# Optimization experiments

Measured on AMD Instinct MI355X. Metric: run time of the kernel, lower is better.

Reference implementation:

```python
import jax, jax.numpy as jnp
import numpy as np

N = 100000      # nodes
E = 1200000     # edges
G = 2048        # graphs in batch
FIN, H, FOUT, K = 75, 16, 64, 3  # in/hidden/out channels, num_stacks


def setup_inputs() -> dict:
    key = jax.random.key(0)
    ks = jax.random.split(key, 12)
    s = 0.1
    return {
        "x": jax.random.normal(ks[0], (N, FIN), jnp.float32),
        "edge_index": jax.random.randint(ks[1], (2, E), 0, N),
        "batch": jnp.sort(jax.random.randint(ks[2], (N,), 0, G)),
        # ARMAConv1 (75 -> 16), shared weights across T=2 layers
        "w1_init": jax.random.normal(ks[3], (K, FIN, H), jnp.float32) * s,
        "w1_w": jax.random.normal(ks[4], (K, H, H), jnp.float32) * s,
        "w1_root": jax.random.normal(ks[5], (K, FIN, H), jnp.float32) * s,
        "w1_bias": jnp.zeros((K, 1, H), jnp.float32),
        # ARMAConv2 (16 -> 64), act=None
        "w2_init": jax.random.normal(ks[6], (K, H, FOUT), jnp.float32) * s,
        "w2_w": jax.random.normal(ks[7], (K, FOUT, FOUT), jnp.float32) * s,
        "w2_root": jax.random.normal(ks[8], (K, H, FOUT), jnp.float32) * s,
        "w2_bias": jnp.zeros((K, 1, FOUT), jnp.float32),
        # gather head Linear(64, 1)
        "wg": jax.random.normal(ks[9], (FOUT, 1), jnp.float32) * s,
        "bg": jnp.zeros((1,), jnp.float32),
    }


def reference(x, edge_index, batch, w1_init, w1_w, w1_root, w1_bias,
              w2_init, w2_w, w2_root, w2_bias, wg, bg):
    row, col = edge_index[0], edge_index[1]
    # gcn_norm without self-loops: deg over target nodes, sym normalization
    deg = jnp.zeros((N,), x.dtype).at[col].add(1.0)
    dinv = jnp.where(deg > 0, deg ** -0.5, 0.0)
    norm = dinv[row] * dinv[col]  # [E]

    def prop(h):  # h: [K, N, F] -> A_norm @ h per stack
        msg = h[:, row, :] * norm[None, :, None]        # [K, E, F]
        return jnp.zeros_like(h).at[:, col, :].add(msg)

    def arma(x0, wi, ww, wr, b, act):
        # x0: [N, Fin]; T=2 layers, shared weights
        out = None
        for t in range(2):
            if t == 0:
                out = jnp.einsum('nf,kfo->kno', x0, wi)   # init transform
            else:
                out = jnp.einsum('kno,kop->knp', out, ww)  # shared weight
            out = prop(out)
            out = out + jnp.einsum('nf,kfo->kno', x0, wr) + b  # root + bias
            if act:
                out = jax.nn.relu(out)
        return out.mean(axis=0)  # average over K stacks -> [N, F]

    h1 = jax.nn.relu(arma(x, w1_init, w1_w, w1_root, w1_bias, True))
    h2 = arma(h1, w2_init, w2_w, w2_root, w2_bias, False)
    # global_add_pool over graph ids, then linear head
    pooled = jnp.zeros((G, h2.shape[-1]), h2.dtype).at[batch].add(h2)
    return pooled @ wg + bg  # [G, 1]
```

## Files before the change

### kernel.cpp

```cpp
#include <hip/hip_runtime.h>

#define NN 100000
#define NE 1200000
#define NG 2048
#define NBK 391
#define CAPQ 4096
#define CAPE 5120

static inline int cdiv(long long a, int b) { return (int)((a + b - 1) / b); }

__device__ __forceinline__ unsigned short f2bf(float f) {
    unsigned int u = __float_as_uint(f);
    u += 0x7fffu + ((u >> 16) & 1u);
    return (unsigned short)(u >> 16);
}
__device__ __forceinline__ unsigned int pack2(float a, float b) {
    return (unsigned int)f2bf(a) | ((unsigned int)f2bf(b) << 16);
}
__device__ __forceinline__ float lo2f(unsigned int w) { return __uint_as_float(w << 16); }
__device__ __forceinline__ float hi2f(unsigned int w) { return __uint_as_float(w & 0xffff0000u); }

__global__ void k_init(int* __restrict__ gcur, uint4* __restrict__ A16,
                       uint4* __restrict__ B16, float2* __restrict__ s12,
                       float* __restrict__ t2, float* __restrict__ dinv) {
    int g = blockIdx.x * blockDim.x + threadIdx.x;
    if (g < NBK) gcur[g] = g * CAPQ;
    if (g == NBK) dinv[NN] = 0.f;
    if (g == NBK + 1) s12[NN] = make_float2(0.f, 0.f);
    if (g == NBK + 2) t2[NN] = 0.f;
    uint4 z = make_uint4(0u, 0u, 0u, 0u);
    int s = g - 512;
    if (s >= 0 && s < 6) {
        A16[(size_t)NN * 6 + s] = z;
        B16[(size_t)NN * 6 + s] = z;
    }
}

__global__ __launch_bounds__(256) void k_part(const int4* __restrict__ row4,
                                              const int4* __restrict__ col4,
                                              int* __restrict__ gcur,
                                              int* __restrict__ pairs, int E4) {
    __shared__ int hcnt[NBK];
    __shared__ int hbase[NBK];
    int chunk = (E4 + gridDim.x - 1) / gridDim.x;
    int beg = blockIdx.x * chunk;
    int end = min(E4, beg + chunk);
    for (int j = threadIdx.x; j < NBK; j += 256) hcnt[j] = 0;
    __syncthreads();
    for (int g = beg + threadIdx.x; g < end; g += 256) {
        int4 c = col4[g];
        atomicAdd(&hcnt[c.x >> 8], 1);
        atomicAdd(&hcnt[c.y >> 8], 1);
        atomicAdd(&hcnt[c.z >> 8], 1);
        atomicAdd(&hcnt[c.w >> 8], 1);
    }
    __syncthreads();
    for (int j = threadIdx.x; j < NBK; j += 256) {
        int c = hcnt[j];
        hbase[j] = c > 0 ? atomicAdd(&gcur[j], c) : 0;
        hcnt[j] = 0;
    }
    __syncthreads();
    for (int g = beg + threadIdx.x; g < end; g += 256) {
        int4 c = col4[g];
        int4 r = row4[g];
        int b0 = c.x >> 8, b1 = c.y >> 8, b2 = c.z >> 8, b3 = c.w >> 8;
        int p0 = hbase[b0] + atomicAdd(&hcnt[b0], 1);
        if (p0 < (b0 + 1) * CAPQ) pairs[p0] = ((c.x & 255) << 17) | r.x;
        int p1 = hbase[b1] + atomicAdd(&hcnt[b1], 1);
        if (p1 < (b1 + 1) * CAPQ) pairs[p1] = ((c.y & 255) << 17) | r.y;
        int p2 = hbase[b2] + atomicAdd(&hcnt[b2], 1);
        if (p2 < (b2 + 1) * CAPQ) pairs[p2] = ((c.z & 255) << 17) | r.z;
        int p3 = hbase[b3] + atomicAdd(&hcnt[b3], 1);
        if (p3 < (b3 + 1) * CAPQ) pairs[p3] = ((c.w & 255) << 17) | r.w;
    }
}

__global__ __launch_bounds__(256) void k_bucket(const int* __restrict__ pairs,
                                                const int* __restrict__ gcur,
                                                int* __restrict__ esrc,
                                                int* __restrict__ rowptrp,
                                                float* __restrict__ dinv, int N) {
    __shared__ int stage[CAPE];
    __shared__ int lcnt[256];
    __shared__ int s[256];
    __shared__ int tot;
    int b = blockIdx.x;
    int base = b << 8;
    int nn = min(256, N - base);
    int qb = b * CAPQ;
    int qe = min(gcur[b], qb + CAPQ);
    int cnt = qe - qb;
    int n4 = cnt >> 2, tail = cnt & 3;
    const int4* pairs4 = (const int4*)(pairs + qb);
    int tid = threadIdx.x;
    lcnt[tid] = 0;
    __syncthreads();
    for (int g = tid; g < n4; g += 256) {
        int4 v = pairs4[g];
        atomicAdd(&lcnt[v.x >> 17], 1);
        atomicAdd(&lcnt[v.y >> 17], 1);
        atomicAdd(&lcnt[v.z >> 17], 1);
        atomicAdd(&lcnt[v.w >> 17], 1);
    }
    if (tid < tail) atomicAdd(&lcnt[pairs[qb + n4 * 4 + tid] >> 17], 1);
    __syncthreads();
    int c = lcnt[tid];
    int pc = (c + 3) & ~3;
    s[tid] = pc;
    __syncthreads();
    for (int off = 1; off < 256; off <<= 1) {
        int t = (tid >= off) ? s[tid - off] : 0;
        __syncthreads();
        s[tid] += t;
        __syncthreads();
    }
    int myofs = s[tid] - pc;
    if (tid == 255) tot = s[255];
    __syncthreads();
    int padded = tot;
    if (tid < nn) {
        dinv[base + tid] = c > 0 ? rsqrtf((float)c) : 0.f;
        rowptrp[base + tid] = ((b * CAPE + myofs) >> 2) | ((pc >> 2) << 20);
    }
    int4* stage4 = (int4*)stage;
    int pad4 = padded >> 2;
    int4 sent = make_int4(N, N, N, N);
    for (int i = tid; i < pad4; i += 256) stage4[i] = sent;
    lcnt[tid] = myofs;
    __syncthreads();
    for (int g = tid; g < n4; g += 256) {
        int4 v = pairs4[g];
        int pos;
        pos = atomicAdd(&lcnt[v.x >> 17], 1); stage[pos] = v.x & 0x1FFFF;
        pos = atomicAdd(&lcnt[v.y >> 17], 1); stage[pos] = v.y & 0x1FFFF;
        pos = atomicAdd(&lcnt[v.z >> 17], 1); stage[pos] = v.z & 0x1FFFF;
        pos = atomicAdd(&lcnt[v.w >> 17], 1); stage[pos] = v.w & 0x1FFFF;
    }
    if (tid < tail) {
        int v = pairs[qb + n4 * 4 + tid];
        int pos = atomicAdd(&lcnt[v >> 17], 1);
        stage[pos] = v & 0x1FFFF;
    }
    __syncthreads();
    int4* esrc4 = (int4*)(esrc + b * CAPE);
    for (int i = tid; i < pad4; i += 256) esrc4[i] = stage4[i];
}

__global__ void k_mmAR(const float* __restrict__ x,
                       const float* __restrict__ w1i, const float* __restrict__ w1r,
                       const float* __restrict__ b1, const float* __restrict__ dinv,
                       ushort4* __restrict__ A16s, float4* __restrict__ R4, int N) {
    __shared__ float4 Wi[900];
    __shared__ float4 Wr[900];
    __shared__ float4 Bs[12];
    const float4* wi4 = (const float4*)w1i;
    const float4* wr4 = (const float4*)w1r;
    for (int i = threadIdx.x; i < 900; i += blockDim.x) { Wi[i] = wi4[i]; Wr[i] = wr4[i]; }
    if (threadIdx.x < 12) Bs[threadIdx.x] = ((const float4*)b1)[threadIdx.x];
    __syncthreads();
    const int total = N * 12;
    const int stride = gridDim.x * blockDim.x;
    for (int idx = blockIdx.x * blockDim.x + threadIdx.x; idx < total; idx += stride) {
        int n = idx / 12;
        int q = idx - n * 12;
        int k = q >> 2, o4 = q & 3;
        const float* xp = x + (size_t)n * 75;
        const float4* wpi = Wi + (k * 75) * 4 + o4;
        const float4* wpr = Wr + (k * 75) * 4 + o4;
        float aix = 0.f, aiy = 0.f, aiz = 0.f, aiw = 0.f;
        float4 br = Bs[q];
        float arx = br.x, ary = br.y, arz = br.z, arw = br.w;
#pragma unroll
        for (int f = 0; f < 75; ++f) {
            float xv = xp[f];
            float4 wi = wpi[f * 4];
            float4 wr = wpr[f * 4];
            aix = fmaf(xv, wi.x, aix);
            aiy = fmaf(xv, wi.y, aiy);
            aiz = fmaf(xv, wi.z, aiz);
            aiw = fmaf(xv, wi.w, aiw);
            arx = fmaf(xv, wr.x, arx);
            ary = fmaf(xv, wr.y, ary);
            arz = fmaf(xv, wr.z, arz);
            arw = fmaf(xv, wr.w, arw);
        }
        float dn = dinv[n];
        ushort4 sa;
        sa.x = f2bf(aix * dn); sa.y = f2bf(aiy * dn);
        sa.z = f2bf(aiz * dn); sa.w = f2bf(aiw * dn);
        A16s[(size_t)n * 12 + q] = sa;
        R4[idx] = make_float4(arx, ary, arz, arw);
    }
}

#define ACC8(W)                                                     \
    a0 += lo2f(W.x); a1 += hi2f(W.x); a2 += lo2f(W.y); a3 += hi2f(W.y); \
    a4 += lo2f(W.z); a5 += hi2f(W.z); a6 += lo2f(W.w); a7 += hi2f(W.w);

template <int HAS_R, int COMPUTE_S, int SCALE_OUT>
__global__ void k_prop48(const uint4* __restrict__ src, const float4* __restrict__ R4,
                         const int* __restrict__ rowptrp, const int* __restrict__ esrc,
                         const float* __restrict__ dinv, float* __restrict__ sv,
                         uint4* __restrict__ dst, int N) {
    const int total = N * 6;
    const int stride = gridDim.x * blockDim.x;
    for (int idx = blockIdx.x * blockDim.x + threadIdx.x; idx < total; idx += stride) {
        int n = idx / 6;
        int q = idx - n * 6;
        int rp = rowptrp[n];
        int beg = (rp & 0xFFFFF) << 2;
        int end = beg + ((rp >> 20) << 2);
        float a0 = 0.f, a1 = 0.f, a2 = 0.f, a3 = 0.f, a4 = 0.f, a5 = 0.f, a6 = 0.f, a7 = 0.f;
        float sd = 0.f;
        int p = beg;
        for (; p + 8 <= end; p += 8) {
            int4 e0 = *(const int4*)(esrc + p);
            int4 e1 = *(const int4*)(esrc + p + 4);
            uint4 w0 = src[(size_t)e0.x * 6 + q];
            uint4 w1 = src[(size_t)e0.y * 6 + q];
            uint4 w2 = src[(size_t)e0.z * 6 + q];
            uint4 w3 = src[(size_t)e0.w * 6 + q];
            uint4 w4 = src[(size_t)e1.x * 6 + q];
            uint4 w5 = src[(size_t)e1.y * 6 + q];
            uint4 w6 = src[(size_t)e1.z * 6 + q];
            uint4 w7 = src[(size_t)e1.w * 6 + q];
            ACC8(w0); ACC8(w1); ACC8(w2); ACC8(w3);
            ACC8(w4); ACC8(w5); ACC8(w6); ACC8(w7);
            if (COMPUTE_S) {
                if (q == 0)
                    sd += ((dinv[e0.x] + dinv[e0.y]) + (dinv[e0.z] + dinv[e0.w]))
                        + ((dinv[e1.x] + dinv[e1.y]) + (dinv[e1.z] + dinv[e1.w]));
            }
        }
        if (p < end) {
            int4 e = *(const int4*)(esrc + p);
            uint4 w0 = src[(size_t)e.x * 6 + q];
            uint4 w1 = src[(size_t)e.y * 6 + q];
            uint4 w2 = src[(size_t)e.z * 6 + q];
            uint4 w3 = src[(size_t)e.w * 6 + q];
            ACC8(w0); ACC8(w1); ACC8(w2); ACC8(w3);
            if (COMPUTE_S) {
                if (q == 0)
                    sd += (dinv[e.x] + dinv[e.y]) + (dinv[e.z] + dinv[e.w]);
            }
        }
        float dn = dinv[n];
        float v0 = a0 * dn, v1 = a1 * dn, v2 = a2 * dn, v3 = a3 * dn;
        float v4 = a4 * dn, v5 = a5 * dn, v6 = a6 * dn, v7 = a7 * dn;
        if (HAS_R) {
            float4 r0 = R4[(size_t)n * 12 + q * 2];
            float4 r1 = R4[(size_t)n * 12 + q * 2 + 1];
            v0 = fmaxf(v0 + r0.x, 0.f); v1 = fmaxf(v1 + r0.y, 0.f);
            v2 = fmaxf(v2 + r0.z, 0.f); v3 = fmaxf(v3 + r0.w, 0.f);
            v4 = fmaxf(v4 + r1.x, 0.f); v5 = fmaxf(v5 + r1.y, 0.f);
            v6 = fmaxf(v6 + r1.z, 0.f); v7 = fmaxf(v7 + r1.w, 0.f);
        }
        if (SCALE_OUT) {
            v0 *= dn; v1 *= dn; v2 *= dn; v3 *= dn;
            v4 *= dn; v5 *= dn; v6 *= dn; v7 *= dn;
        }
        uint4 o;
        o.x = pack2(v0, v1); o.y = pack2(v2, v3);
        o.z = pack2(v4, v5); o.w = pack2(v6, v7);
        dst[(size_t)n * 6 + q] = o;
        if (COMPUTE_S) {
            if (q == 0) sv[n] = sd * dn;
        }
    }
}

__global__ void k_post1(const uint4* __restrict__ A16, const float4* __restrict__ R4,
                        const float* __restrict__ w1w, const float* __restrict__ dinv,
                        const float* __restrict__ u,
                        float* __restrict__ z0, float2* __restrict__ s12, int N) {
    __shared__ float4 Ws[192];
    const float4* w4 = (const float4*)w1w;
    for (int i = threadIdx.x; i < 192; i += blockDim.x) Ws[i] = w4[i];
    __syncthreads();
    const int total = N * 4;
    const int stride = gridDim.x * blockDim.x;
    for (int idx = blockIdx.x * blockDim.x + threadIdx.x; idx < total; idx += stride) {
        int n = idx >> 2;
        int o4 = idx & 3;
        const uint4* ap = A16 + (size_t)n * 6;
        float av[48];
#pragma unroll
        for (int c6 = 0; c6 < 6; ++c6) {
            uint4 w = ap[c6];
            av[c6 * 8 + 0] = lo2f(w.x); av[c6 * 8 + 1] = hi2f(w.x);
            av[c6 * 8 + 2] = lo2f(w.y); av[c6 * 8 + 3] = hi2f(w.y);
            av[c6 * 8 + 4] = lo2f(w.z); av[c6 * 8 + 5] = hi2f(w.z);
            av[c6 * 8 + 6] = lo2f(w.w); av[c6 * 8 + 7] = hi2f(w.w);
        }
        float4 sum = make_float4(0.f, 0.f, 0.f, 0.f);
#pragma unroll
        for (int k = 0; k < 3; ++k) {
            float4 d = R4[(size_t)n * 12 + k * 4 + o4];
#pragma unroll
            for (int i = 0; i < 16; ++i) {
                float a = av[k * 16 + i];
                float4 w = Ws[(k * 16 + i) * 4 + o4];
                d.x = fmaf(a, w.x, d.x);
                d.y = fmaf(a, w.y, d.y);
                d.z = fmaf(a, w.z, d.z);
                d.w = fmaf(a, w.w, d.w);
            }
            d.x = fmaxf(d.x, 0.f); d.y = fmaxf(d.y, 0.f);
            d.z = fmaxf(d.z, 0.f); d.w = fmaxf(d.w, 0.f);
            sum.x += d.x; sum.y += d.y; sum.z += d.z; sum.w += d.w;
        }
        const float third = 1.0f / 3.0f;
        sum.x *= third; sum.y *= third; sum.z *= third; sum.w *= third;
        float4 u0q = ((const float4*)u)[o4];
        float4 u1q = ((const float4*)u)[4 + o4];
        float4 u2q = ((const float4*)u)[8 + o4];
        float d0 = sum.x * u0q.x + sum.y * u0q.y + sum.z * u0q.z + sum.w * u0q.w;
        float d1 = sum.x * u1q.x + sum.y * u1q.y + sum.z * u1q.z + sum.w * u1q.w;
        float d2 = sum.x * u2q.x + sum.y * u2q.y + sum.z * u2q.z + sum.w * u2q.w;
        d0 += __shfl_down(d0, 2, 4); d0 += __shfl_down(d0, 1, 4);
        d1 += __shfl_down(d1, 2, 4); d1 += __shfl_down(d1, 1, 4);
        d2 += __shfl_down(d2, 2, 4); d2 += __shfl_down(d2, 1, 4);
        if (o4 == 0) {
            float dn = dinv[n];
            z0[n] = d0;
            s12[n] = make_float2(d1 * dn, d2 * dn);
        }
    }
}

__global__ void k_passA(const float2* __restrict__ s12,
                        const int* __restrict__ rowptrp, const int* __restrict__ esrc,
                        const float* __restrict__ dinv, const float* __restrict__ z0,
                        float* __restrict__ z01, float* __restrict__ t2, int N) {
    int n = blockIdx.x * blockDim.x + threadIdx.x;
    if (n >= N) return;
    int rp = rowptrp[n];
    int beg = (rp & 0xFFFFF) << 2;
    int end = beg + ((rp >> 20) << 2);
    float S1 = 0.f, S2 = 0.f;
    int p = beg;
    for (; p + 8 <= end; p += 8) {
        int4 e0 = *(const int4*)(esrc + p);
        int4 e1 = *(const int4*)(esrc + p + 4);
        float2 v0 = s12[e0.x], v1 = s12[e0.y], v2 = s12[e0.z], v3 = s12[e0.w];
        float2 v4 = s12[e1.x], v5 = s12[e1.y], v6 = s12[e1.z], v7 = s12[e1.w];
        S1 += ((v0.x + v1.x) + (v2.x + v3.x)) + ((v4.x + v5.x) + (v6.x + v7.x));
        S2 += ((v0.y + v1.y) + (v2.y + v3.y)) + ((v4.y + v5.y) + (v6.y + v7.y));
    }
    if (p < end) {
        int4 e = *(const int4*)(esrc + p);
        float2 v0 = s12[e.x], v1 = s12[e.y], v2 = s12[e.z], v3 = s12[e.w];
        S1 += (v0.x + v1.x) + (v2.x + v3.x);
        S2 += (v0.y + v1.y) + (v2.y + v3.y);
    }
    float dn = dinv[n];
    z01[n] = z0[n] + dn * S1;
    t2[n] = dn * dn * S2;
}

__global__ void k_passB(const float* __restrict__ t2,
                        const int* __restrict__ rowptrp, const int* __restrict__ esrc,
                        const float* __restrict__ dinv, const float* __restrict__ z01,
                        const float* __restrict__ sv, const float* __restrict__ u,
                        const int* __restrict__ batch, float* __restrict__ out, int N) {
    int n = blockIdx.x * blockDim.x + threadIdx.x;
    if (n >= N) return;
    int rp = rowptrp[n];
    int beg = (rp & 0xFFFFF) << 2;
    int end = beg + ((rp >> 20) << 2);
    float S = 0.f;
    int p = beg;
    for (; p + 8 <= end; p += 8) {
        int4 e0 = *(const int4*)(esrc + p);
        int4 e1 = *(const int4*)(esrc + p + 4);
        S += ((t2[e0.x] + t2[e0.y]) + (t2[e0.z] + t2[e0.w]))
           + ((t2[e1.x] + t2[e1.y]) + (t2[e1.z] + t2[e1.w]));
    }
    if (p < end) {
        int4 e = *(const int4*)(esrc + p);
        S += (t2[e.x] + t2[e.y]) + (t2[e.z] + t2[e.w]);
    }
    float v = z01[n] + dinv[n] * S + sv[n] * u[48] + u[49];
    atomicAdd(&out[batch[n]], v);
}

__global__ void k_comb(const float* __restrict__ w2i, const float* __restrict__ w2w,
                       const float* __restrict__ w2r, const float* __restrict__ b2,
                       const float* __restrict__ wg, const float* __restrict__ bg,
                       float* __restrict__ u, float* __restrict__ out) {
    if (blockIdx.x > 0) {
        int g = (blockIdx.x - 1) * 256 + threadIdx.x;
        if (g < NG) out[g] = bg[0];
        return;
    }
    __shared__ float t[3][64];
    int tid = threadIdx.x;
    if (tid < 64) {
#pragma unroll
        for (int k = 0; k < 3; ++k) {
            float a = 0.f;
            for (int j = 0; j < 64; ++j) a = fmaf(w2w[k * 4096 + tid * 64 + j], wg[j], a);
            t[k][tid] = a;
        }
    }
    __syncthreads();
    if (tid < 64) {
        float wgv = wg[tid];
        float tk0 = t[0][tid], tk1 = t[1][tid], tk2 = t[2][tid];
        const float third = 1.0f / 3.0f;
        for (int j = 0; j < 16; ++j) {
            float wi0 = w2i[j * 64 + tid], wi1 = w2i[1024 + j * 64 + tid], wi2 = w2i[2048 + j * 64 + tid];
            float wr0 = w2r[j * 64 + tid], wr1 = w2r[1024 + j * 64 + tid], wr2 = w2r[2048 + j * 64 + tid];
            float a2 = wi0 * tk0 + wi1 * tk1 + wi2 * tk2;
            float a1 = wr0 * tk0 + wr1 * tk1 + wr2 * tk2;
            float a0 = (wr0 + wr1 + wr2) * wgv;
#pragma unroll
            for (int off = 32; off > 0; off >>= 1) {
                a2 += __shfl_down(a2, off, 64);
                a1 += __shfl_down(a1, off, 64);
                a0 += __shfl_down(a0, off, 64);
            }
            if (tid == 0) {
                u[j] = a0 * third;
                u[16 + j] = a1 * third;
                u[32 + j] = a2 * third;
            }
        }
        float b0 = b2[tid], b1v = b2[64 + tid], b2v = b2[128 + tid];
        float c0 = b0 * tk0 + b1v * tk1 + b2v * tk2;
        float c1 = (b0 + b1v + b2v) * wgv;
#pragma unroll
        for (int off = 32; off > 0; off >>= 1) {
            c0 += __shfl_down(c0, off, 64);
            c1 += __shfl_down(c1, off, 64);
        }
        if (tid == 0) {
            u[48] = c0 * third;
            u[49] = c1 * third;
        }
    }
}

extern "C" void kernel_launch(void* const* d_in, const int* in_sizes, int n_in,
                              void* d_out, int out_size, void* d_ws, size_t ws_size,
                              hipStream_t stream) {
    const float* x   = (const float*)d_in[0];
    const int*   ei  = (const int*)d_in[1];
    const int*   batch = (const int*)d_in[2];
    const float* w1i = (const float*)d_in[3];
    const float* w1w = (const float*)d_in[4];
    const float* w1r = (const float*)d_in[5];
    const float* w1b = (const float*)d_in[6];
    const float* w2i = (const float*)d_in[7];
    const float* w2w = (const float*)d_in[8];
    const float* w2r = (const float*)d_in[9];
    const float* w2b = (const float*)d_in[10];
    const float* wg  = (const float*)d_in[11];
    const float* bg  = (const float*)d_in[12];
    float* out = (float*)d_out;

    uint4*  A16  = (uint4*)d_ws;
    uint4*  B16  = A16 + (size_t)(NN + 1) * 6;
    float*  R    = (float*)(B16 + (size_t)(NN + 1) * 6);
    float2* s12  = (float2*)(R + (size_t)NN * 48);
    float*  t2   = (float*)(s12 + NN + 1);
    float*  z0   = t2 + NN + 1;
    float*  z01  = z0 + NN;
    float*  dinv = z01 + NN;
    float*  sv   = dinv + NN + 1;
    float*  u    = sv + NN;
    int* rowptrp = (int*)(u + 64);
    int* gcur    = rowptrp + NN;
    int* pairs   = gcur + 512;
    int* esrc    = pairs + (size_t)(NBK + 1) * CAPQ;

    const int T = 256;

    k_init<<<3, T, 0, stream>>>(gcur, A16, B16, s12, t2, dinv);
    k_part<<<512, T, 0, stream>>>((const int4*)ei, (const int4*)(ei + NE),
                                  gcur, pairs, NE / 4);
    k_bucket<<<NBK, T, 0, stream>>>(pairs, gcur, esrc, rowptrp, dinv, NN);

    k_comb<<<9, T, 0, stream>>>(w2i, w2w, w2r, w2b, wg, bg, u, out);

    k_mmAR<<<2048, T, 0, stream>>>(x, w1i, w1r, w1b, dinv, (ushort4*)A16, (float4*)R, NN);

    k_prop48<1, 1, 1><<<cdiv((long long)NN * 6, T), T, 0, stream>>>(
        A16, (const float4*)R, rowptrp, esrc, dinv, sv, B16, NN);
    k_prop48<0, 0, 0><<<cdiv((long long)NN * 6, T), T, 0, stream>>>(
        B16, nullptr, rowptrp, esrc, dinv, nullptr, A16, NN);
    k_post1<<<cdiv((long long)NN * 4, T), T, 0, stream>>>(
        A16, (const float4*)R, w1w, dinv, u, z0, s12, NN);

    k_passA<<<cdiv(NN, T), T, 0, stream>>>(s12, rowptrp, esrc, dinv, z0, z01, t2, NN);
    k_passB<<<cdiv(NN, T), T, 0, stream>>>(t2, rowptrp, esrc, dinv, z01, sv, u, batch, out, NN);
}
```

Before: 203.0 us.

## Store root term in bf16 and fuse second propagation with post-transform

```diff
diff --git a/kernel.cpp b/kernel.cpp
--- a/kernel.cpp
+++ b/kernel.cpp
@@ -6,6 +6,7 @@
 #define NBK 391
 #define CAPQ 4096
 #define CAPE 5120
+#define NPB 42
 
 static inline int cdiv(long long a, int b) { return (int)((a + b - 1) / b); }
 
@@ -14,8 +15,8 @@
     u += 0x7fffu + ((u >> 16) & 1u);
     return (unsigned short)(u >> 16);
 }
-__device__ __forceinline__ unsigned int pack2(float a, float b) {
-    return (unsigned int)f2bf(a) | ((unsigned int)f2bf(b) << 16);
+__device__ __forceinline__ float bf2f(unsigned short h) {
+    return __uint_as_float((unsigned int)h << 16);
 }
 __device__ __forceinline__ float lo2f(unsigned int w) { return __uint_as_float(w << 16); }
 __device__ __forceinline__ float hi2f(unsigned int w) { return __uint_as_float(w & 0xffff0000u); }
@@ -150,7 +151,7 @@
 __global__ void k_mmAR(const float* __restrict__ x,
                        const float* __restrict__ w1i, const float* __restrict__ w1r,
                        const float* __restrict__ b1, const float* __restrict__ dinv,
-                       ushort4* __restrict__ A16s, float4* __restrict__ R4, int N) {
+                       ushort4* __restrict__ A16s, ushort4* __restrict__ R16s, int N) {
     __shared__ float4 Wi[900];
     __shared__ float4 Wr[900];
     __shared__ float4 Bs[12];
@@ -190,7 +191,10 @@
         sa.x = f2bf(aix * dn); sa.y = f2bf(aiy * dn);
         sa.z = f2bf(aiz * dn); sa.w = f2bf(aiw * dn);
         A16s[(size_t)n * 12 + q] = sa;
-        R4[idx] = make_float4(arx, ary, arz, arw);
+        ushort4 sr;
+        sr.x = f2bf(arx); sr.y = f2bf(ary);
+        sr.z = f2bf(arz); sr.w = f2bf(arw);
+        R16s[(size_t)n * 12 + q] = sr;
     }
 }
 
@@ -198,8 +202,7 @@
     a0 += lo2f(W.x); a1 += hi2f(W.x); a2 += lo2f(W.y); a3 += hi2f(W.y); \
     a4 += lo2f(W.z); a5 += hi2f(W.z); a6 += lo2f(W.w); a7 += hi2f(W.w);
 
-template <int HAS_R, int COMPUTE_S, int SCALE_OUT>
-__global__ void k_prop48(const uint4* __restrict__ src, const float4* __restrict__ R4,
+__global__ void k_prop48(const uint4* __restrict__ src, const uint4* __restrict__ R16,
                          const int* __restrict__ rowptrp, const int* __restrict__ esrc,
                          const float* __restrict__ dinv, float* __restrict__ sv,
                          uint4* __restrict__ dst, int N) {
@@ -227,11 +230,9 @@
             uint4 w7 = src[(size_t)e1.w * 6 + q];
             ACC8(w0); ACC8(w1); ACC8(w2); ACC8(w3);
             ACC8(w4); ACC8(w5); ACC8(w6); ACC8(w7);
-            if (COMPUTE_S) {
-                if (q == 0)
-                    sd += ((dinv[e0.x] + dinv[e0.y]) + (dinv[e0.z] + dinv[e0.w]))
-                        + ((dinv[e1.x] + dinv[e1.y]) + (dinv[e1.z] + dinv[e1.w]));
-            }
+            if (q == 0)
+                sd += ((dinv[e0.x] + dinv[e0.y]) + (dinv[e0.z] + dinv[e0.w]))
+                    + ((dinv[e1.x] + dinv[e1.y]) + (dinv[e1.z] + dinv[e1.w]));
         }
         if (p < end) {
             int4 e = *(const int4*)(esrc + p);
@@ -240,91 +241,118 @@
             uint4 w2 = src[(size_t)e.z * 6 + q];
             uint4 w3 = src[(size_t)e.w * 6 + q];
             ACC8(w0); ACC8(w1); ACC8(w2); ACC8(w3);
-            if (COMPUTE_S) {
-                if (q == 0)
-                    sd += (dinv[e.x] + dinv[e.y]) + (dinv[e.z] + dinv[e.w]);
+            if (q == 0)
+                sd += (dinv[e.x] + dinv[e.y]) + (dinv[e.z] + dinv[e.w]);
+        }
+        float dn = dinv[n];
+        uint4 r = R16[(size_t)n * 6 + q];
+        float v0 = fmaxf(a0 * dn + lo2f(r.x), 0.f) * dn;
+        float v1 = fmaxf(a1 * dn + hi2f(r.x), 0.f) * dn;
+        float v2 = fmaxf(a2 * dn + lo2f(r.y), 0.f) * dn;
+        float v3 = fmaxf(a3 * dn + hi2f(r.y), 0.f) * dn;
+        float v4 = fmaxf(a4 * dn + lo2f(r.z), 0.f) * dn;
+        float v5 = fmaxf(a5 * dn + hi2f(r.z), 0.f) * dn;
+        float v6 = fmaxf(a6 * dn + lo2f(r.w), 0.f) * dn;
+        float v7 = fmaxf(a7 * dn + hi2f(r.w), 0.f) * dn;
+        uint4 o;
+        o.x = (unsigned)f2bf(v0) | ((unsigned)f2bf(v1) << 16);
+        o.y = (unsigned)f2bf(v2) | ((unsigned)f2bf(v3) << 16);
+        o.z = (unsigned)f2bf(v4) | ((unsigned)f2bf(v5) << 16);
+        o.w = (unsigned)f2bf(v6) | ((unsigned)f2bf(v7) << 16);
+        dst[(size_t)n * 6 + q] = o;
+        if (q == 0) sv[n] = sd * dn;
+    }
+}
+
+__global__ __launch_bounds__(256) void k_proppost(
+    const uint4* __restrict__ B16, const ushort4* __restrict__ R16s,
+    const float* __restrict__ w1w, const int* __restrict__ rowptrp,
+    const int* __restrict__ esrc, const float* __restrict__ dinv,
+    const float* __restrict__ u, float* __restrict__ z0,
+    float2* __restrict__ s12, int N) {
+    __shared__ float4 Ws[192];
+    __shared__ float ash[NPB][48];
+    const float4* w4 = (const float4*)w1w;
+    for (int i = threadIdx.x; i < 192; i += 256) Ws[i] = w4[i];
+    int t = threadIdx.x;
+    int nbase = blockIdx.x * NPB;
+    if (t < NPB * 6) {
+        int ln = t / 6, q = t - ln * 6;
+        int n = nbase + ln;
+        if (n < N) {
+            int rp = rowptrp[n];
+            int beg = (rp & 0xFFFFF) << 2;
+            int end = beg + ((rp >> 20) << 2);
+            float a0 = 0.f, a1 = 0.f, a2 = 0.f, a3 = 0.f, a4 = 0.f, a5 = 0.f, a6 = 0.f, a7 = 0.f;
+            int p = beg;
+            for (; p + 8 <= end; p += 8) {
+                int4 e0 = *(const int4*)(esrc + p);
+                int4 e1 = *(const int4*)(esrc + p + 4);
+                uint4 w0 = B16[(size_t)e0.x * 6 + q];
+                uint4 w1 = B16[(size_t)e0.y * 6 + q];
+                uint4 w2 = B16[(size_t)e0.z * 6 + q];
+                uint4 w3 = B16[(size_t)e0.w * 6 + q];
+                uint4 w4v = B16[(size_t)e1.x * 6 + q];
+                uint4 w5 = B16[(size_t)e1.y * 6 + q];
+                uint4 w6 = B16[(size_t)e1.z * 6 + q];
+                uint4 w7 = B16[(size_t)e1.w * 6 + q];
+                ACC8(w0); ACC8(w1); ACC8(w2); ACC8(w3);
+                ACC8(w4v); ACC8(w5); ACC8(w6); ACC8(w7);
             }
-        }
-        float dn = dinv[n];
-        float v0 = a0 * dn, v1 = a1 * dn, v2 = a2 * dn, v3 = a3 * dn;
-        float v4 = a4 * dn, v5 = a5 * dn, v6 = a6 * dn, v7 = a7 * dn;
-        if (HAS_R) {
-            float4 r0 = R4[(size_t)n * 12 + q * 2];
-            float4 r1 = R4[(size_t)n * 12 + q * 2 + 1];
-            v0 = fmaxf(v0 + r0.x, 0.f); v1 = fmaxf(v1 + r0.y, 0.f);
-            v2 = fmaxf(v2 + r0.z, 0.f); v3 = fmaxf(v3 + r0.w, 0.f);
-            v4 = fmaxf(v4 + r1.x, 0.f); v5 = fmaxf(v5 + r1.y, 0.f);
-            v6 = fmaxf(v6 + r1.z, 0.f); v7 = fmaxf(v7 + r1.w, 0.f);
-        }
-        if (SCALE_OUT) {
-            v0 *= dn; v1 *= dn; v2 *= dn; v3 *= dn;
-            v4 *= dn; v5 *= dn; v6 *= dn; v7 *= dn;
-        }
-        uint4 o;
-        o.x = pack2(v0, v1); o.y = pack2(v2, v3);
-        o.z = pack2(v4, v5); o.w = pack2(v6, v7);
-        dst[(size_t)n * 6 + q] = o;
-        if (COMPUTE_S) {
-            if (q == 0) sv[n] = sd * dn;
-        }
-    }
-}
-
-__global__ void k_post1(const uint4* __restrict__ A16, const float4* __restrict__ R4,
-                        const float* __restrict__ w1w, const float* __restrict__ dinv,
-                        const float* __restrict__ u,
-                        float* __restrict__ z0, float2* __restrict__ s12, int N) {
-    __shared__ float4 Ws[192];
-    const float4* w4 = (const float4*)w1w;
-    for (int i = threadIdx.x; i < 192; i += blockDim.x) Ws[i] = w4[i];
-    __syncthreads();
-    const int total = N * 4;
-    const int stride = gridDim.x * blockDim.x;
-    for (int idx = blockIdx.x * blockDim.x + threadIdx.x; idx < total; idx += stride) {
-        int n = idx >> 2;
-        int o4 = idx & 3;
-        const uint4* ap = A16 + (size_t)n * 6;
-        float av[48];
+            if (p < end) {
+                int4 e = *(const int4*)(esrc + p);
+                uint4 w0 = B16[(size_t)e.x * 6 + q];
+                uint4 w1 = B16[(size_t)e.y * 6 + q];
+                uint4 w2 = B16[(size_t)e.z * 6 + q];
+                uint4 w3 = B16[(size_t)e.w * 6 + q];
+                ACC8(w0); ACC8(w1); ACC8(w2); ACC8(w3);
+            }
+            float dn = dinv[n];
+            float* ap = &ash[ln][q * 8];
+            ap[0] = a0 * dn; ap[1] = a1 * dn; ap[2] = a2 * dn; ap[3] = a3 * dn;
+            ap[4] = a4 * dn; ap[5] = a5 * dn; ap[6] = a6 * dn; ap[7] = a7 * dn;
+        }
+    }
+    __syncthreads();
+    if (t < NPB * 4) {
+        int ln = t >> 2, o4 = t & 3;
+        int n = nbase + ln;
+        if (n < N) {
+            float4 sum = make_float4(0.f, 0.f, 0.f, 0.f);
 #pragma unroll
-        for (int c6 = 0; c6 < 6; ++c6) {
-            uint4 w = ap[c6];
-            av[c6 * 8 + 0] = lo2f(w.x); av[c6 * 8 + 1] = hi2f(w.x);
-            av[c6 * 8 + 2] = lo2f(w.y); av[c6 * 8 + 3] = hi2f(w.y);
-            av[c6 * 8 + 4] = lo2f(w.z); av[c6 * 8 + 5] = hi2f(w.z);
-            av[c6 * 8 + 6] = lo2f(w.w); av[c6 * 8 + 7] = hi2f(w.w);
-        }
-        float4 sum = make_float4(0.f, 0.f, 0.f, 0.f);
+            for (int k = 0; k < 3; ++k) {
+                ushort4 rq = R16s[(size_t)n * 12 + k * 4 + o4];
+                float4 d;
+                d.x = bf2f(rq.x); d.y = bf2f(rq.y); d.z = bf2f(rq.z); d.w = bf2f(rq.w);
 #pragma unroll
-        for (int k = 0; k < 3; ++k) {
-            float4 d = R4[(size_t)n * 12 + k * 4 + o4];
-#pragma unroll
-            for (int i = 0; i < 16; ++i) {
-                float a = av[k * 16 + i];
-                float4 w = Ws[(k * 16 + i) * 4 + o4];
-                d.x = fmaf(a, w.x, d.x);
-                d.y = fmaf(a, w.y, d.y);
-                d.z = fmaf(a, w.z, d.z);
-                d.w = fmaf(a, w.w, d.w);
+                for (int i = 0; i < 16; ++i) {
+                    float a = ash[ln][k * 16 + i];
+                    float4 w = Ws[(k * 16 + i) * 4 + o4];
+                    d.x = fmaf(a, w.x, d.x);
+                    d.y = fmaf(a, w.y, d.y);
+                    d.z = fmaf(a, w.z, d.z);
+                    d.w = fmaf(a, w.w, d.w);
+                }
+                d.x = fmaxf(d.x, 0.f); d.y = fmaxf(d.y, 0.f);
+                d.z = fmaxf(d.z, 0.f); d.w = fmaxf(d.w, 0.f);
+                sum.x += d.x; sum.y += d.y; sum.z += d.z; sum.w += d.w;
             }
-            d.x = fmaxf(d.x, 0.f); d.y = fmaxf(d.y, 0.f);
-            d.z = fmaxf(d.z, 0.f); d.w = fmaxf(d.w, 0.f);
-            sum.x += d.x; sum.y += d.y; sum.z += d.z; sum.w += d.w;
-        }
-        const float third = 1.0f / 3.0f;
-        sum.x *= third; sum.y *= third; sum.z *= third; sum.w *= third;
-        float4 u0q = ((const float4*)u)[o4];
-        float4 u1q = ((const float4*)u)[4 + o4];
-        float4 u2q = ((const float4*)u)[8 + o4];
-        float d0 = sum.x * u0q.x + sum.y * u0q.y + sum.z * u0q.z + sum.w * u0q.w;
-        float d1 = sum.x * u1q.x + sum.y * u1q.y + sum.z * u1q.z + sum.w * u1q.w;
-        float d2 = sum.x * u2q.x + sum.y * u2q.y + sum.z * u2q.z + sum.w * u2q.w;
-        d0 += __shfl_down(d0, 2, 4); d0 += __shfl_down(d0, 1, 4);
-        d1 += __shfl_down(d1, 2, 4); d1 += __shfl_down(d1, 1, 4);
-        d2 += __shfl_down(d2, 2, 4); d2 += __shfl_down(d2, 1, 4);
-        if (o4 == 0) {
-            float dn = dinv[n];
-            z0[n] = d0;
-            s12[n] = make_float2(d1 * dn, d2 * dn);
+            const float third = 1.0f / 3.0f;
+            sum.x *= third; sum.y *= third; sum.z *= third; sum.w *= third;
+            float4 u0q = ((const float4*)u)[o4];
+            float4 u1q = ((const float4*)u)[4 + o4];
+            float4 u2q = ((const float4*)u)[8 + o4];
+            float d0 = sum.x * u0q.x + sum.y * u0q.y + sum.z * u0q.z + sum.w * u0q.w;
+            float d1 = sum.x * u1q.x + sum.y * u1q.y + sum.z * u1q.z + sum.w * u1q.w;
+            float d2 = sum.x * u2q.x + sum.y * u2q.y + sum.z * u2q.z + sum.w * u2q.w;
+            d0 += __shfl_down(d0, 2, 4); d0 += __shfl_down(d0, 1, 4);
+            d1 += __shfl_down(d1, 2, 4); d1 += __shfl_down(d1, 1, 4);
+            d2 += __shfl_down(d2, 2, 4); d2 += __shfl_down(d2, 1, 4);
+            if (o4 == 0) {
+                float dn = dinv[n];
+                z0[n] = d0;
+                s12[n] = make_float2(d1 * dn, d2 * dn);
+            }
         }
     }
 }
@@ -462,8 +490,8 @@
 
     uint4*  A16  = (uint4*)d_ws;
     uint4*  B16  = A16 + (size_t)(NN + 1) * 6;
-    float*  R    = (float*)(B16 + (size_t)(NN + 1) * 6);
-    float2* s12  = (float2*)(R + (size_t)NN * 48);
+    uint4*  R16  = B16 + (size_t)(NN + 1) * 6;
+    float2* s12  = (float2*)(R16 + (size_t)NN * 6);
     float*  t2   = (float*)(s12 + NN + 1);
     float*  z0   = t2 + NN + 1;
     float*  z01  = z0 + NN;
@@ -484,14 +512,14 @@
 
     k_comb<<<9, T, 0, stream>>>(w2i, w2w, w2r, w2b, wg, bg, u, out);
 
-    k_mmAR<<<2048, T, 0, stream>>>(x, w1i, w1r, w1b, dinv, (ushort4*)A16, (float4*)R, NN);
-
-    k_prop48<1, 1, 1><<<cdiv((long long)NN * 6, T), T, 0, stream>>>(
-        A16, (const float4*)R, rowptrp, esrc, dinv, sv, B16, NN);
-    k_prop48<0, 0, 0><<<cdiv((long long)NN * 6, T), T, 0, stream>>>(
-        B16, nullptr, rowptrp, esrc, dinv, nullptr, A16, NN);
-    k_post1<<<cdiv((long long)NN * 4, T), T, 0, stream>>>(
-        A16, (const float4*)R, w1w, dinv, u, z0, s12, NN);
+    k_mmAR<<<2048, T, 0, stream>>>(x, w1i, w1r, w1b, dinv,
+                                   (ushort4*)A16, (ushort4*)R16, NN);
+
+    k_prop48<<<cdiv((long long)NN * 6, T), T, 0, stream>>>(
+        A16, R16, rowptrp, esrc, dinv, sv, B16, NN);
+
+    k_proppost<<<cdiv(NN, NPB), T, 0, stream>>>(
+        B16, (const ushort4*)R16, w1w, rowptrp, esrc, dinv, u, z0, s12, NN);
 
     k_passA<<<cdiv(NN, T), T, 0, stream>>>(s12, rowptrp, esrc, dinv, z0, z01, t2, NN);
     k_passB<<<cdiv(NN, T), T, 0, stream>>>(t2, rowptrp, esrc, dinv, z01, sv, u, batch, out, NN);
```

New measurement: 193.5 us. 4.7% less time.
